# Kernel optimization log

Measured on AMD Instinct MI355X. Metric: run time of the kernel, lower is better.

Reference implementation:

```python
import jax, jax.numpy as jnp
import numpy as np

V = 32000   # vocab
D = 512     # embed dim
H = 512     # hidden dim
K = 5       # beam size
SOS, EOS, PAD = 0, 1, 2
NEG = -1e30  # acts as -inf but keeps grads NaN-free


def gru_cell(x, h, Wih, Whh, bih, bhh):
    # torch nn.GRU cell convention: gates ordered (r, z, n)
    gi = x @ Wih.T + bih
    gh = h @ Whh.T + bhh
    i_r, i_z, i_n = jnp.split(gi, 3, axis=-1)
    h_r, h_z, h_n = jnp.split(gh, 3, axis=-1)
    r = jax.nn.sigmoid(i_r + h_r)
    z = jax.nn.sigmoid(i_z + h_z)
    n = jnp.tanh(i_n + r * h_n)
    return (1.0 - z) * n + z * h


def setup_inputs() -> dict:
    key = jax.random.key(0)
    ks = jax.random.split(key, 14)
    s = 0.02
    f = jnp.float32
    return {
        "source": jax.random.randint(ks[0], (32, 32), 0, V, dtype=jnp.int32),
        "emb_src": jax.random.normal(ks[1], (V, D), f) * s,
        "emb_tgt": jax.random.normal(ks[2], (V, D), f) * s,
        "enc_Wih": jax.random.normal(ks[3], (3 * H, D), f) * s,
        "enc_Whh": jax.random.normal(ks[4], (3 * H, H), f) * s,
        "enc_bih": jnp.zeros((3 * H,), f),
        "enc_bhh": jnp.zeros((3 * H,), f),
        "dec_Wih": jax.random.normal(ks[5], (3 * H, D), f) * s,
        "dec_Whh": jax.random.normal(ks[6], (3 * H, H), f) * s,
        "dec_bih": jnp.zeros((3 * H,), f),
        "dec_bhh": jnp.zeros((3 * H,), f),
        "W_out": jax.random.normal(ks[7], (H, V), f) * s,
        "b_out": jnp.zeros((V,), f),
    }


def beam_search(source, emb_src, emb_tgt, enc_Wih, enc_Whh, enc_bih, enc_bhh,
                dec_Wih, dec_Whh, dec_bih, dec_bhh, W_out, b_out):
    B, S = source.shape
    T = S + 1  # max decode steps (while counter < source.shape[1] + 1)

    # ---- encoder: 1-layer GRU over source tokens ----
    xs = jnp.swapaxes(emb_src[source], 0, 1)  # [S, B, D]
    def enc_step(h, x):
        return gru_cell(x, h, enc_Wih, enc_Whh, enc_bih, enc_bhh), None
    h_enc, _ = jax.lax.scan(enc_step, jnp.zeros((B, H), xs.dtype), xs)
    # initialize_h: repeat each sentence's hidden state beam_size times
    hidden = jnp.broadcast_to(h_enc[:, None, :], (B, K, H))  # [B, K, H]

    def dec_logprobs(tok, hid):
        x = emb_tgt[tok]  # [B, K, D]
        h1 = gru_cell(x, hid, dec_Wih, dec_Whh, dec_bih, dec_bhh)
        lp = jax.nn.log_softmax(h1 @ W_out + b_out, axis=-1)  # [B, K, V]
        return lp, h1

    # ---- step 0: initial_advance (top-K words from one SOS row) ----
    lp, h1 = dec_logprobs(jnp.zeros((B, K), jnp.int32), hidden)
    vals, words = jax.lax.top_k(lp[:, 0, :], K)  # [B, K]
    seqs = jnp.full((B, K, T + 1), PAD, jnp.int32)
    seqs = seqs.at[:, :, 0].set(SOS).at[:, :, 1].set(words)
    act_ll = vals
    hidden = h1  # all beams identical at step 0
    best_ll = jnp.full((B,), NEG, vals.dtype)
    best_seq = jnp.full((B, T + 1), PAD, jnp.int32)
    pos = jnp.arange(T + 1)
    bidx = jnp.arange(B)

    # ---- steps 1..T-1: advance. Dead beam slots carry NEG likelihood,
    # which reproduces the shrinking-active-set math of the original. ----
    def step(carry, t):
        seqs, act_ll, hidden, last_tok, best_ll, best_seq = carry
        lp, h1 = dec_logprobs(last_tok, hidden)
        L = (act_ll[:, :, None] + lp).reshape(B, K * V)
        vals, idx = jax.lax.top_k(L, K)
        parent = idx // V           # seq_ind
        word = idx % V              # word_ind
        gathered = jnp.take_along_axis(seqs, parent[:, :, None], axis=1)
        new_seqs = jnp.where(pos[None, None, :] == t + 1, word[:, :, None], gathered)
        finite = vals > NEG * 0.5
        is_eos = (word == EOS) & finite
        # completed likelihood normalized by candidate length (t+2 tokens)
        comp_ll = jnp.where(is_eos, vals / (t.astype(vals.dtype) + 2.0), NEG)
        cbest = comp_ll.max(axis=1)
        cseq = new_seqs[bidx, comp_ll.argmax(axis=1)]  # [B, T+1], PAD-padded
        improve = cbest > best_ll
        best_ll = jnp.where(improve, cbest, best_ll)
        best_seq = jnp.where(improve[:, None], cseq, best_seq)
        act_ll = jnp.where(finite & ~is_eos, vals, NEG)
        hidden = jnp.take_along_axis(h1, parent[:, :, None], axis=1)  # arrange_h gather
        return (new_seqs, act_ll, hidden, word, best_ll, best_seq), None

    carry = (seqs, act_ll, hidden, words, best_ll, best_seq)
    carry, _ = jax.lax.scan(step, carry, jnp.arange(1, T))
    seqs, act_ll, hidden, last_tok, best_ll, best_seq = carry

    # return_winner: best completed if any, else best active
    have = best_ll > NEG * 0.5
    act_best = act_ll.argmax(axis=1)
    act_seq = seqs[bidx, act_best]
    winner = jnp.where(have[:, None], best_seq, act_seq)  # [B, T+1]
    winner_ll = jnp.where(have, best_ll, act_ll.max(axis=1))
    return winner, winner_ll


def reference(source, emb_src, emb_tgt, enc_Wih, enc_Whh, enc_bih, enc_bhh,
              dec_Wih, dec_Whh, dec_bih, dec_bhh, W_out, b_out):
    winner, _ = beam_search(source, emb_src, emb_tgt, enc_Wih, enc_Whh, enc_bih,
                            enc_bhh, dec_Wih, dec_Whh, dec_bih, dec_bhh, W_out, b_out)
    return winner
```

## Files before the change

kernel.cpp:

```cpp
#include <hip/hip_runtime.h>
#include <math.h>

#define NEGF   (-1e30f)
#define FINTH  (-5e29f)
#define VSZ    32000
#define KBM    5
#define SEQL   34
#define NVBLK  1000

__device__ __forceinline__ bool cand_gt(float av, int ai, float bv, int bi) {
  return (av > bv) || (av == bv && ai < bi);
}

#define INS5(xx, ii)                                                           \
  if (cand_gt(xx, ii, tv4, ti4)) {                                             \
    tv4 = xx; ti4 = ii;                                                        \
    if (cand_gt(tv4, ti4, tv3, ti3)) { float tf = tv3; int tj = ti3; tv3 = tv4; ti3 = ti4; tv4 = tf; ti4 = tj; \
      if (cand_gt(tv3, ti3, tv2, ti2)) { tf = tv2; tj = ti2; tv2 = tv3; ti2 = ti3; tv3 = tf; ti3 = tj; \
        if (cand_gt(tv2, ti2, tv1, ti1)) { tf = tv1; tj = ti1; tv1 = tv2; ti1 = ti2; tv2 = tf; ti2 = tj; \
          if (cand_gt(tv1, ti1, tv0, ti0)) { tf = tv0; tj = ti0; tv0 = tv1; ti0 = ti1; tv1 = tf; ti1 = tj; } } } } }

__global__ void init_kernel(float* hb0, int* word_buf, int* hsrc) {
  int i = blockIdx.x * 256 + threadIdx.x;
  if (i < 32 * 512) hb0[i] = 0.f;
  if (i < 160) { word_buf[i] = 0; hsrc[i] = i / KBM; }
}

__global__ __launch_bounds__(256, 4) void genc_kernel(
    const float* __restrict__ emb, const int* __restrict__ source,
    const float* __restrict__ Wih, float* __restrict__ gi_enc)
{
  const int tid = threadIdx.x;
  const int ng = tid & 7;
  const int mg = tid >> 3;
  const int j0 = blockIdx.x * 16 + ng * 2;
  const int r0 = blockIdx.y * 128 + mg * 4;

  const float* arow[4];
  #pragma unroll
  for (int i = 0; i < 4; i++) {
    int r = r0 + i;
    int tok = source[(r & 31) * 32 + (r >> 5)];
    arow[i] = emb + (long)tok * 512;
  }
  const float* w0p = Wih + (long)j0 * 512;
  const float* w1p = w0p + 512;

  float acc0[4], acc1[4];
  #pragma unroll
  for (int i = 0; i < 4; i++) { acc0[i] = 0.f; acc1[i] = 0.f; }

  float4 wc0 = *(const float4*)w0p;
  float4 wc1 = *(const float4*)w1p;
  float4 ac[4];
  #pragma unroll
  for (int i = 0; i < 4; i++) ac[i] = *(const float4*)arow[i];

  for (int k = 0; k < 508; k += 4) {
    float4 wn0 = *(const float4*)(w0p + k + 4);
    float4 wn1 = *(const float4*)(w1p + k + 4);
    float4 an[4];
    #pragma unroll
    for (int i = 0; i < 4; i++) an[i] = *(const float4*)(arow[i] + k + 4);
    #pragma unroll
    for (int i = 0; i < 4; i++) {
      acc0[i] += ac[i].x * wc0.x + ac[i].y * wc0.y + ac[i].z * wc0.z + ac[i].w * wc0.w;
      acc1[i] += ac[i].x * wc1.x + ac[i].y * wc1.y + ac[i].z * wc1.z + ac[i].w * wc1.w;
    }
    wc0 = wn0; wc1 = wn1;
    #pragma unroll
    for (int i = 0; i < 4; i++) ac[i] = an[i];
  }
  #pragma unroll
  for (int i = 0; i < 4; i++) {
    acc0[i] += ac[i].x * wc0.x + ac[i].y * wc0.y + ac[i].z * wc0.z + ac[i].w * wc0.w;
    acc1[i] += ac[i].x * wc1.x + ac[i].y * wc1.y + ac[i].z * wc1.z + ac[i].w * wc1.w;
  }
  #pragma unroll
  for (int i = 0; i < 4; i++) {
    float2 r; r.x = acc0[i]; r.y = acc1[i];
    *(float2*)(gi_enc + (long)(r0 + i) * 1536 + j0) = r;
  }
}

template<int P, int HONLY>
__global__ __launch_bounds__(256, 4) void gates_kernel(
    const float* __restrict__ emb, const int* __restrict__ tok_ptr, int tok_stride,
    const float* __restrict__ hbuf, const int* __restrict__ hsrc,
    const float* __restrict__ Wih, const float* __restrict__ Whh,
    float* __restrict__ gip, float* __restrict__ ghp)
{
  const bool is_h = HONLY ? true : (blockIdx.y != 0);
  const float* W = is_h ? Whh : Wih;
  const int M = 32 * P;
  float* out = (is_h ? ghp : gip) + (long)blockIdx.z * M * 1536;

  const int tid = threadIdx.x;
  const int ng = tid & 7;
  const int mg = tid >> 3;
  const int j0 = blockIdx.x * 16 + ng * 2;
  const int k0 = blockIdx.z * 128;

  const float* arow[P];
  #pragma unroll
  for (int i = 0; i < P; i++) {
    int m = mg * P + i;
    if (is_h) { int r = hsrc ? hsrc[m] : m; arow[i] = hbuf + (long)r * 512 + k0; }
    else      { int tk = tok_ptr[m * tok_stride]; arow[i] = emb + (long)tk * 512 + k0; }
  }
  const float* w0p = W + (long)j0 * 512 + k0;
  const float* w1p = w0p + 512;

  float acc0[P], acc1[P];
  #pragma unroll
  for (int i = 0; i < P; i++) { acc0[i] = 0.f; acc1[i] = 0.f; }

  float4 wc0 = *(const float4*)w0p;
  float4 wc1 = *(const float4*)w1p;
  float4 ac[P];
  #pragma unroll
  for (int i = 0; i < P; i++) ac[i] = *(const float4*)arow[i];

  for (int k = 0; k < 124; k += 4) {
    float4 wn0 = *(const float4*)(w0p + k + 4);
    float4 wn1 = *(const float4*)(w1p + k + 4);
    float4 an[P];
    #pragma unroll
    for (int i = 0; i < P; i++) an[i] = *(const float4*)(arow[i] + k + 4);
    #pragma unroll
    for (int i = 0; i < P; i++) {
      acc0[i] += ac[i].x * wc0.x + ac[i].y * wc0.y + ac[i].z * wc0.z + ac[i].w * wc0.w;
      acc1[i] += ac[i].x * wc1.x + ac[i].y * wc1.y + ac[i].z * wc1.z + ac[i].w * wc1.w;
    }
    wc0 = wn0; wc1 = wn1;
    #pragma unroll
    for (int i = 0; i < P; i++) ac[i] = an[i];
  }
  #pragma unroll
  for (int i = 0; i < P; i++) {
    acc0[i] += ac[i].x * wc0.x + ac[i].y * wc0.y + ac[i].z * wc0.z + ac[i].w * wc0.w;
    acc1[i] += ac[i].x * wc1.x + ac[i].y * wc1.y + ac[i].z * wc1.z + ac[i].w * wc1.w;
  }
  #pragma unroll
  for (int i = 0; i < P; i++) {
    int m = mg * P + i;
    float2 r; r.x = acc0[i]; r.y = acc1[i];
    *(float2*)(out + (long)m * 1536 + j0) = r;
  }
}

template<int NPI, int NPH, int M>
__global__ __launch_bounds__(256) void hupd_kernel(
    const float* __restrict__ gip, const float* __restrict__ ghp,
    const float* __restrict__ bih, const float* __restrict__ bhh,
    const float* __restrict__ hin, const int* __restrict__ hsrc,
    float* __restrict__ hout)
{
  int idx = blockIdx.x * 256 + threadIdx.x;
  if (idx >= M * 512) return;
  int m = idx >> 9, i = idx & 511;
  float ir = 0.f, iz = 0.f, inn = 0.f, hr = 0.f, hz = 0.f, hn = 0.f;
  #pragma unroll
  for (int p = 0; p < NPI; p++) {
    const float* g = gip + (long)p * M * 1536 + (long)m * 1536;
    ir += g[i]; iz += g[512 + i]; inn += g[1024 + i];
  }
  #pragma unroll
  for (int p = 0; p < NPH; p++) {
    const float* g = ghp + (long)p * M * 1536 + (long)m * 1536;
    hr += g[i]; hz += g[512 + i]; hn += g[1024 + i];
  }
  ir += bih[i]; iz += bih[512 + i]; inn += bih[1024 + i];
  hr += bhh[i]; hz += bhh[512 + i]; hn += bhh[1024 + i];
  float r = 1.f / (1.f + expf(-(ir + hr)));
  float z = 1.f / (1.f + expf(-(iz + hz)));
  float n = tanhf(inn + r * hn);
  int src = hsrc ? hsrc[m] : m;
  float h = hin[(long)src * 512 + i];
  hout[(long)m * 512 + i] = (1.f - z) * n + z * h;
}

__global__ __launch_bounds__(256, 4) void logtop_kernel(
    const float* __restrict__ h1, const float* __restrict__ Wout,
    const float* __restrict__ bout,
    float* __restrict__ pms, float* __restrict__ pv, int* __restrict__ pi)
{
  const int tid = threadIdx.x;
  const int ng = tid & 7;
  const int mg = tid >> 3;
  const int blk = blockIdx.x;
  const int v = blk * 32 + ng * 4;
  const int m0 = mg * 5;

  const float* a0 = h1 + (long)m0 * 512;
  const float* wp = Wout + v;

  float4 acc[5];
  #pragma unroll
  for (int i = 0; i < 5; i++) acc[i] = make_float4(0.f, 0.f, 0.f, 0.f);

  float4 wc[4], ac[5];
  #pragma unroll
  for (int j = 0; j < 4; j++) wc[j] = *(const float4*)(wp + (long)j * VSZ);
  #pragma unroll
  for (int i = 0; i < 5; i++) ac[i] = *(const float4*)(a0 + i * 512);

  for (int k = 0; k < 508; k += 4) {
    float4 wn[4], an[5];
    #pragma unroll
    for (int j = 0; j < 4; j++) wn[j] = *(const float4*)(wp + (long)(k + 4 + j) * VSZ);
    #pragma unroll
    for (int i = 0; i < 5; i++) an[i] = *(const float4*)(a0 + i * 512 + k + 4);
    #pragma unroll
    for (int i = 0; i < 5; i++) {
      acc[i].x += ac[i].x * wc[0].x + ac[i].y * wc[1].x + ac[i].z * wc[2].x + ac[i].w * wc[3].x;
      acc[i].y += ac[i].x * wc[0].y + ac[i].y * wc[1].y + ac[i].z * wc[2].y + ac[i].w * wc[3].y;
      acc[i].z += ac[i].x * wc[0].z + ac[i].y * wc[1].z + ac[i].z * wc[2].z + ac[i].w * wc[3].z;
      acc[i].w += ac[i].x * wc[0].w + ac[i].y * wc[1].w + ac[i].z * wc[2].w + ac[i].w * wc[3].w;
    }
    #pragma unroll
    for (int j = 0; j < 4; j++) wc[j] = wn[j];
    #pragma unroll
    for (int i = 0; i < 5; i++) ac[i] = an[i];
  }
  #pragma unroll
  for (int i = 0; i < 5; i++) {
    acc[i].x += ac[i].x * wc[0].x + ac[i].y * wc[1].x + ac[i].z * wc[2].x + ac[i].w * wc[3].x;
    acc[i].y += ac[i].x * wc[0].y + ac[i].y * wc[1].y + ac[i].z * wc[2].y + ac[i].w * wc[3].y;
    acc[i].z += ac[i].x * wc[0].z + ac[i].y * wc[1].z + ac[i].z * wc[2].z + ac[i].w * wc[3].z;
    acc[i].w += ac[i].x * wc[0].w + ac[i].y * wc[1].w + ac[i].z * wc[2].w + ac[i].w * wc[3].w;
  }

  __shared__ float L[160][33];
  float4 bb = *(const float4*)(bout + v);
  #pragma unroll
  for (int i = 0; i < 5; i++) {
    L[m0 + i][ng * 4 + 0] = acc[i].x + bb.x;
    L[m0 + i][ng * 4 + 1] = acc[i].y + bb.y;
    L[m0 + i][ng * 4 + 2] = acc[i].z + bb.z;
    L[m0 + i][ng * 4 + 3] = acc[i].w + bb.w;
  }
  __syncthreads();

  if (tid < 160) {
    float m = -3.4e38f, s = 0.f;
    float tv0 = -3.4e38f, tv1 = -3.4e38f, tv2 = -3.4e38f, tv3 = -3.4e38f, tv4 = -3.4e38f;
    int ti0 = 0x7fffffff, ti1 = 0x7fffffff, ti2 = 0x7fffffff, ti3 = 0x7fffffff, ti4 = 0x7fffffff;
    int base = blk * 32;
    for (int c = 0; c < 32; c++) {
      float x = L[tid][c];
      if (x > m) { s *= expf(m - x); m = x; }
      s += expf(x - m);
      INS5(x, base + c);
    }
    long o = (long)blk * 160 + tid;
    pms[o * 2 + 0] = m; pms[o * 2 + 1] = s;
    pv[o * 5 + 0] = tv0; pi[o * 5 + 0] = ti0;
    pv[o * 5 + 1] = tv1; pi[o * 5 + 1] = ti1;
    pv[o * 5 + 2] = tv2; pi[o * 5 + 2] = ti2;
    pv[o * 5 + 3] = tv3; pi[o * 5 + 3] = ti3;
    pv[o * 5 + 4] = tv4; pi[o * 5 + 4] = ti4;
  }
}

__global__ __launch_bounds__(256) void merge_kernel(
    const float* __restrict__ pms, const float* __restrict__ pv,
    const int* __restrict__ pi, float* __restrict__ lse,
    float* __restrict__ rv5, int* __restrict__ ri5)
{
  int row = blockIdx.x, tid = threadIdx.x;
  float m = -3.4e38f, s = 0.f;
  float tv0 = -3.4e38f, tv1 = -3.4e38f, tv2 = -3.4e38f, tv3 = -3.4e38f, tv4 = -3.4e38f;
  int ti0 = 0x7fffffff, ti1 = 0x7fffffff, ti2 = 0x7fffffff, ti3 = 0x7fffffff, ti4 = 0x7fffffff;

  for (int blk = tid; blk < NVBLK; blk += 256) {
    long o = (long)blk * 160 + row;
    float bm = pms[o * 2 + 0], bs = pms[o * 2 + 1];
    float nm = fmaxf(m, bm);
    s = s * expf(m - nm) + bs * expf(bm - nm);
    m = nm;
    float xv; int xi;
    xv = pv[o * 5 + 0]; xi = pi[o * 5 + 0]; INS5(xv, xi);
    xv = pv[o * 5 + 1]; xi = pi[o * 5 + 1]; INS5(xv, xi);
    xv = pv[o * 5 + 2]; xi = pi[o * 5 + 2]; INS5(xv, xi);
    xv = pv[o * 5 + 3]; xi = pi[o * 5 + 3]; INS5(xv, xi);
    xv = pv[o * 5 + 4]; xi = pi[o * 5 + 4]; INS5(xv, xi);
  }
  for (int mask = 1; mask < 64; mask <<= 1) {
    float om = __shfl_xor(m, mask, 64);
    float os = __shfl_xor(s, mask, 64);
    float nm = fmaxf(m, om);
    s = s * expf(m - nm) + os * expf(om - nm);
    m = nm;
  }
  __shared__ float sm[4], ss[4];
  __shared__ float sv[256 * 5];
  __shared__ int   si[256 * 5];
  if ((tid & 63) == 0) { sm[tid >> 6] = m; ss[tid >> 6] = s; }
  sv[tid * 5 + 0] = tv0; si[tid * 5 + 0] = ti0;
  sv[tid * 5 + 1] = tv1; si[tid * 5 + 1] = ti1;
  sv[tid * 5 + 2] = tv2; si[tid * 5 + 2] = ti2;
  sv[tid * 5 + 3] = tv3; si[tid * 5 + 3] = ti3;
  sv[tid * 5 + 4] = tv4; si[tid * 5 + 4] = ti4;
  __syncthreads();
  if (tid == 0) {
    float M2 = sm[0], S2 = ss[0];
    for (int w = 1; w < 4; w++) {
      float nm = fmaxf(M2, sm[w]);
      S2 = S2 * expf(M2 - nm) + ss[w] * expf(sm[w] - nm);
      M2 = nm;
    }
    lse[row] = M2 + logf(S2);
  }
  for (int str = 128; str >= 1; str >>= 1) {
    if (tid < str) {
      float* av = &sv[tid * 5];         int* ai = &si[tid * 5];
      float* bv = &sv[(tid + str) * 5]; int* bi = &si[(tid + str) * 5];
      float o0[5]; int o1[5];
      int i = 0, j = 0;
      #pragma unroll
      for (int o = 0; o < 5; o++) {
        float avv = av[i]; int aii = ai[i];
        float bvv = bv[j]; int bii = bi[j];
        bool ta = cand_gt(avv, aii, bvv, bii);
        o0[o] = ta ? avv : bvv; o1[o] = ta ? aii : bii;
        i += ta ? 1 : 0; j += ta ? 0 : 1;
      }
      #pragma unroll
      for (int o = 0; o < 5; o++) { av[o] = o0[o]; ai[o] = o1[o]; }
    }
    __syncthreads();
  }
  if (tid == 0) {
    #pragma unroll
    for (int o = 0; o < 5; o++) { rv5[row * 5 + o] = sv[o]; ri5[row * 5 + o] = si[o]; }
  }
}

__global__ void book0_kernel(const float* __restrict__ rv5, const int* __restrict__ ri5,
                             const float* __restrict__ lse,
                             int* __restrict__ seqs, float* __restrict__ act_ll,
                             int* __restrict__ word_buf, int* __restrict__ hsrc,
                             float* __restrict__ best_ll, int* __restrict__ best_seq)
{
  int b = blockIdx.x, tid = threadIdx.x;
  int row = b * KBM;
  float l = lse[row];
  if (tid < SEQL) {
    for (int j = 0; j < KBM; j++) {
      int w = ri5[row * 5 + j];
      seqs[(b * KBM + j) * SEQL + tid] = (tid == 0) ? 0 : (tid == 1 ? w : 2);
    }
    best_seq[b * SEQL + tid] = 2;
  }
  if (tid < KBM) {
    act_ll[b * KBM + tid] = rv5[row * 5 + tid] - l;
    word_buf[b * KBM + tid] = ri5[row * 5 + tid];
    hsrc[b * KBM + tid] = b * KBM + tid;
  }
  if (tid == 0) best_ll[b] = NEGF;
}

__global__ void book_kernel(const float* __restrict__ rv5, const int* __restrict__ ri5,
                            const float* __restrict__ lse,
                            const int* __restrict__ seqs_old, int* __restrict__ seqs_new,
                            float* __restrict__ act_ll, int* __restrict__ word_buf,
                            int* __restrict__ hsrc, float* __restrict__ best_ll,
                            int* __restrict__ best_seq, int t)
{
  int b = blockIdx.x, tid = threadIdx.x;
  __shared__ float sv5[5];
  __shared__ int   si5[5];
  if (tid == 0) {
    float tv0 = -3.4e38f, tv1 = -3.4e38f, tv2 = -3.4e38f, tv3 = -3.4e38f, tv4 = -3.4e38f;
    int ti0 = 0x7fffffff, ti1 = 0x7fffffff, ti2 = 0x7fffffff, ti3 = 0x7fffffff, ti4 = 0x7fffffff;
    for (int k = 0; k < KBM; k++) {
      int row = b * KBM + k;
      float a = act_ll[row], l = lse[row];
      #pragma unroll
      for (int j = 0; j < 5; j++) {
        float x = a + (rv5[row * 5 + j] - l);
        int id = k * VSZ + ri5[row * 5 + j];
        INS5(x, id);
      }
    }
    sv5[0] = tv0; si5[0] = ti0; sv5[1] = tv1; si5[1] = ti1;
    sv5[2] = tv2; si5[2] = ti2; sv5[3] = tv3; si5[3] = ti3;
    sv5[4] = tv4; si5[4] = ti4;
  }
  __syncthreads();

  __shared__ int ls[KBM][SEQL];
  float v[KBM]; int pr[KBM], wd[KBM];
  #pragma unroll
  for (int j = 0; j < KBM; j++) {
    v[j] = sv5[j];
    int id = si5[j];
    pr[j] = id / VSZ; wd[j] = id % VSZ;
  }
  #pragma unroll
  for (int j = 0; j < KBM; j++) {
    if (tid < SEQL) {
      int x = (tid == t + 1) ? wd[j] : seqs_old[(b * KBM + pr[j]) * SEQL + tid];
      ls[j][tid] = x;
      seqs_new[(b * KBM + j) * SEQL + tid] = x;
    }
  }
  __syncthreads();
  float cll[KBM];
  #pragma unroll
  for (int j = 0; j < KBM; j++) {
    bool fin = v[j] > FINTH;
    bool eos = (wd[j] == 1) && fin;
    cll[j] = eos ? v[j] / (float)(t + 2) : NEGF;
  }
  int jb = 0; float cb = cll[0];
  #pragma unroll
  for (int j = 1; j < KBM; j++) if (cll[j] > cb) { cb = cll[j]; jb = j; }
  bool improve = cb > best_ll[b];
  if (improve) {
    if (tid == 0) best_ll[b] = cb;
    if (tid < SEQL) best_seq[b * SEQL + tid] = ls[jb][tid];
  }
  if (tid < KBM) {
    int j = tid;
    bool fin = v[j] > FINTH;
    bool eos = (wd[j] == 1) && fin;
    act_ll[b * KBM + j] = (fin && !eos) ? v[j] : NEGF;
    word_buf[b * KBM + j] = wd[j];
    hsrc[b * KBM + j] = b * KBM + pr[j];
  }
}

__global__ void final_kernel(const float* __restrict__ best_ll, const int* __restrict__ best_seq,
                             const float* __restrict__ act_ll, const int* __restrict__ seqs,
                             int* __restrict__ out)
{
  int b = blockIdx.x, tid = threadIdx.x;
  bool have = best_ll[b] > FINTH;
  int jb = 0; float ab = act_ll[b * KBM];
  for (int j = 1; j < KBM; j++)
    if (act_ll[b * KBM + j] > ab) { ab = act_ll[b * KBM + j]; jb = j; }
  if (tid < SEQL)
    out[b * SEQL + tid] = have ? best_seq[b * SEQL + tid]
                               : seqs[(b * KBM + jb) * SEQL + tid];
}

extern "C" void kernel_launch(void* const* d_in, const int* in_sizes, int n_in,
                              void* d_out, int out_size, void* d_ws, size_t ws_size,
                              hipStream_t stream)
{
  const int*   source  = (const int*)d_in[0];
  const float* emb_src = (const float*)d_in[1];
  const float* emb_tgt = (const float*)d_in[2];
  const float* eWih = (const float*)d_in[3];
  const float* eWhh = (const float*)d_in[4];
  const float* ebih = (const float*)d_in[5];
  const float* ebhh = (const float*)d_in[6];
  const float* dWih = (const float*)d_in[7];
  const float* dWhh = (const float*)d_in[8];
  const float* dbih = (const float*)d_in[9];
  const float* dbhh = (const float*)d_in[10];
  const float* Wout = (const float*)d_in[11];
  const float* bout = (const float*)d_in[12];
  int* out = (int*)d_out;

  char* ws = (char*)d_ws;
  size_t off = 0;
  auto alloc = [&](size_t bytes) {
    void* p = ws + off;
    off = (off + bytes + 255) & ~(size_t)255;
    return p;
  };
  float* hb0     = (float*)alloc(160 * 512 * 4);
  float* hb1     = (float*)alloc(160 * 512 * 4);
  float* gip     = (float*)alloc((size_t)4 * 160 * 1536 * 4);
  float* ghp     = (float*)alloc((size_t)4 * 160 * 1536 * 4);
  char*  uni     = (char*) alloc((size_t)8 * 1024 * 1024);
  float* gi_enc  = (float*)uni;
  float* pms     = (float*)uni;
  float* pv      = (float*)(uni + 1536 * 1024);
  int*   pi      = (int*)  (uni + 1536 * 1024 + 3328 * 1024);
  float* lse     = (float*)alloc(160 * 4);
  float* act_ll  = (float*)alloc(160 * 4);
  float* rv5     = (float*)alloc(160 * 5 * 4);
  float* best_ll = (float*)alloc(32 * 4);
  int*   ri5     = (int*)alloc(160 * 5 * 4);
  int*   seqs0   = (int*)alloc(160 * SEQL * 4);
  int*   seqs1   = (int*)alloc(160 * SEQL * 4);
  int*   wordb   = (int*)alloc(160 * 4);
  int*   hsrc    = (int*)alloc(160 * 4);
  int*   bseq    = (int*)alloc(32 * SEQL * 4);

  init_kernel<<<64, 256, 0, stream>>>(hb0, wordb, hsrc);

  genc_kernel<<<dim3(96, 8), 256, 0, stream>>>(emb_src, source, eWih, gi_enc);
  for (int s = 0; s < 32; s++) {
    gates_kernel<1, 1><<<dim3(96, 1, 4), 256, 0, stream>>>(
        nullptr, nullptr, 0, hb0, nullptr, nullptr, eWhh, nullptr, ghp);
    hupd_kernel<1, 4, 32><<<64, 256, 0, stream>>>(
        gi_enc + (size_t)s * 32 * 1536, ghp, ebih, ebhh, hb0, nullptr, hb0);
  }

  gates_kernel<5, 0><<<dim3(96, 2, 4), 256, 0, stream>>>(
      emb_tgt, wordb, 1, hb0, hsrc, dWih, dWhh, gip, ghp);
  hupd_kernel<4, 4, 160><<<320, 256, 0, stream>>>(
      gip, ghp, dbih, dbhh, hb0, hsrc, hb1);
  logtop_kernel<<<NVBLK, 256, 0, stream>>>(hb1, Wout, bout, pms, pv, pi);
  merge_kernel<<<160, 256, 0, stream>>>(pms, pv, pi, lse, rv5, ri5);
  book0_kernel<<<32, 64, 0, stream>>>(rv5, ri5, lse, seqs0, act_ll, wordb, hsrc,
                                      best_ll, bseq);

  float* hcur = hb1; float* hoth = hb0;
  int* scur = seqs0; int* soth = seqs1;
  for (int t = 1; t <= 32; t++) {
    gates_kernel<5, 0><<<dim3(96, 2, 4), 256, 0, stream>>>(
        emb_tgt, wordb, 1, hcur, hsrc, dWih, dWhh, gip, ghp);
    hupd_kernel<4, 4, 160><<<320, 256, 0, stream>>>(
        gip, ghp, dbih, dbhh, hcur, hsrc, hoth);
    logtop_kernel<<<NVBLK, 256, 0, stream>>>(hoth, Wout, bout, pms, pv, pi);
    merge_kernel<<<160, 256, 0, stream>>>(pms, pv, pi, lse, rv5, ri5);
    book_kernel<<<32, 64, 0, stream>>>(rv5, ri5, lse, scur, soth, act_ll, wordb,
                                       hsrc, best_ll, bseq, t);
    { float* tmp = hcur; hcur = hoth; hoth = tmp; }
    { int* tmp = scur; scur = soth; soth = tmp; }
  }

  final_kernel<<<32, 64, 0, stream>>>(best_ll, bseq, act_ll, scur, out);
}
```

Measured before the change: 8.174 ms.

## Stage W_out tiles into LDS via async global_load_lds with double buffering

Reworks the logits matmul so W_out tiles (64 rows x 32 columns) are copied straight from global memory into a double-buffered shared-memory region with global_load_lds, instead of each thread loading its own float4 weight rows into registers. Threads then read the weights from LDS, while the activation rows are still prefetched from global with a two-step register ping-pong. The aim is to cut redundant global weight traffic across the 20 threads that share columns and to overlap the next tile's load with compute. In exchange it adds LDS use and a barrier per tile, which may lower occupancy. It also relies on the loads having completed by the time the barrier passes, with no explicit wait on the async copy.

```diff
diff --git a/kernel.cpp b/kernel.cpp
--- a/kernel.cpp
+++ b/kernel.cpp
@@ -189,56 +189,85 @@
   const int ng = tid & 7;
   const int mg = tid >> 3;
   const int blk = blockIdx.x;
-  const int v = blk * 32 + ng * 4;
+  const int v0 = blk * 32;
+  const int v = v0 + ng * 4;
   const int m0 = mg * 5;
 
+  __shared__ float Wlds[2][2048];
+  __shared__ float L[160][33];
+
   const float* a0 = h1 + (long)m0 * 512;
-  const float* wp = Wout + v;
+
+  const int skk = tid >> 3;
+  const int sv4 = tid & 7;
+  const float* sg0 = Wout + (size_t)skk * VSZ + v0 + sv4 * 4;
+  const float* sg1 = Wout + (size_t)(32 + skk) * VSZ + v0 + sv4 * 4;
+  const int lwave = (tid >> 6) * 256;
+
+  auto stage = [&](int tt, int bb) {
+    const float* g0 = sg0 + (size_t)tt * 64 * VSZ;
+    const float* g1 = sg1 + (size_t)tt * 64 * VSZ;
+    __builtin_amdgcn_global_load_lds(
+        (const __attribute__((address_space(1))) void*)g0,
+        (__attribute__((address_space(3))) void*)&Wlds[bb][lwave], 16, 0, 0);
+    __builtin_amdgcn_global_load_lds(
+        (const __attribute__((address_space(1))) void*)g1,
+        (__attribute__((address_space(3))) void*)&Wlds[bb][1024 + lwave], 16, 0, 0);
+  };
 
   float4 acc[5];
   #pragma unroll
   for (int i = 0; i < 5; i++) acc[i] = make_float4(0.f, 0.f, 0.f, 0.f);
 
-  float4 wc[4], ac[5];
-  #pragma unroll
-  for (int j = 0; j < 4; j++) wc[j] = *(const float4*)(wp + (long)j * VSZ);
-  #pragma unroll
-  for (int i = 0; i < 5; i++) ac[i] = *(const float4*)(a0 + i * 512);
-
-  for (int k = 0; k < 508; k += 4) {
-    float4 wn[4], an[5];
-    #pragma unroll
-    for (int j = 0; j < 4; j++) wn[j] = *(const float4*)(wp + (long)(k + 4 + j) * VSZ);
-    #pragma unroll
-    for (int i = 0; i < 5; i++) an[i] = *(const float4*)(a0 + i * 512 + k + 4);
-    #pragma unroll
-    for (int i = 0; i < 5; i++) {
-      acc[i].x += ac[i].x * wc[0].x + ac[i].y * wc[1].x + ac[i].z * wc[2].x + ac[i].w * wc[3].x;
-      acc[i].y += ac[i].x * wc[0].y + ac[i].y * wc[1].y + ac[i].z * wc[2].y + ac[i].w * wc[3].y;
-      acc[i].z += ac[i].x * wc[0].z + ac[i].y * wc[1].z + ac[i].z * wc[2].z + ac[i].w * wc[3].z;
-      acc[i].w += ac[i].x * wc[0].w + ac[i].y * wc[1].w + ac[i].z * wc[2].w + ac[i].w * wc[3].w;
-    }
-    #pragma unroll
-    for (int j = 0; j < 4; j++) wc[j] = wn[j];
-    #pragma unroll
-    for (int i = 0; i < 5; i++) ac[i] = an[i];
-  }
+  stage(0, 0);
+  __syncthreads();
+
+  float4 aA[5], aB[5];
+  #pragma unroll
+  for (int i = 0; i < 5; i++) aA[i] = *(const float4*)(a0 + i * 512);
+
+  for (int t8 = 0; t8 < 8; t8++) {
+    const float* lb = &Wlds[t8 & 1][0];
+    if (t8 < 7) stage(t8 + 1, (t8 + 1) & 1);
+    const int kt = t8 * 64;
+    #pragma unroll 1
+    for (int c = 0; c < 16; c += 2) {
+      const int k = kt + c * 4;
+      float4 w0[4], w1[4];
+      #pragma unroll
+      for (int j = 0; j < 4; j++) w0[j] = *(const float4*)&lb[(c * 4 + j) * 32 + ng * 4];
+      #pragma unroll
+      for (int j = 0; j < 4; j++) w1[j] = *(const float4*)&lb[(c * 4 + 4 + j) * 32 + ng * 4];
+      #pragma unroll
+      for (int i = 0; i < 5; i++) aB[i] = *(const float4*)(a0 + i * 512 + k + 4);
+      #pragma unroll
+      for (int i = 0; i < 5; i++) {
+        acc[i].x += aA[i].x * w0[0].x + aA[i].y * w0[1].x + aA[i].z * w0[2].x + aA[i].w * w0[3].x;
+        acc[i].y += aA[i].x * w0[0].y + aA[i].y * w0[1].y + aA[i].z * w0[2].y + aA[i].w * w0[3].y;
+        acc[i].z += aA[i].x * w0[0].z + aA[i].y * w0[1].z + aA[i].z * w0[2].z + aA[i].w * w0[3].z;
+        acc[i].w += aA[i].x * w0[0].w + aA[i].y * w0[1].w + aA[i].z * w0[2].w + aA[i].w * w0[3].w;
+      }
+      int kn = k + 8; if (kn >= 512) kn = 0;
+      #pragma unroll
+      for (int i = 0; i < 5; i++) aA[i] = *(const float4*)(a0 + i * 512 + kn);
+      #pragma unroll
+      for (int i = 0; i < 5; i++) {
+        acc[i].x += aB[i].x * w1[0].x + aB[i].y * w1[1].x + aB[i].z * w1[2].x + aB[i].w * w1[3].x;
+        acc[i].y += aB[i].x * w1[0].y + aB[i].y * w1[1].y + aB[i].z * w1[2].y + aB[i].w * w1[3].y;
+        acc[i].z += aB[i].x * w1[0].z + aB[i].y * w1[1].z + aB[i].z * w1[2].z + aB[i].w * w1[3].z;
+        acc[i].w += aB[i].x * w1[0].w + aB[i].y * w1[1].w + aB[i].z * w1[2].w + aB[i].w * w1[3].w;
+      }
+    }
+    __syncthreads();
+  }
+
+  float4 bb4 = *(const float4*)(bout + v);
   #pragma unroll
   for (int i = 0; i < 5; i++) {
-    acc[i].x += ac[i].x * wc[0].x + ac[i].y * wc[1].x + ac[i].z * wc[2].x + ac[i].w * wc[3].x;
-    acc[i].y += ac[i].x * wc[0].y + ac[i].y * wc[1].y + ac[i].z * wc[2].y + ac[i].w * wc[3].y;
-    acc[i].z += ac[i].x * wc[0].z + ac[i].y * wc[1].z + ac[i].z * wc[2].z + ac[i].w * wc[3].z;
-    acc[i].w += ac[i].x * wc[0].w + ac[i].y * wc[1].w + ac[i].z * wc[2].w + ac[i].w * wc[3].w;
-  }
-
-  __shared__ float L[160][33];
-  float4 bb = *(const float4*)(bout + v);
-  #pragma unroll
-  for (int i = 0; i < 5; i++) {
-    L[m0 + i][ng * 4 + 0] = acc[i].x + bb.x;
-    L[m0 + i][ng * 4 + 1] = acc[i].y + bb.y;
-    L[m0 + i][ng * 4 + 2] = acc[i].z + bb.z;
-    L[m0 + i][ng * 4 + 3] = acc[i].w + bb.w;
+    L[m0 + i][ng * 4 + 0] = acc[i].x + bb4.x;
+    L[m0 + i][ng * 4 + 1] = acc[i].y + bb4.y;
+    L[m0 + i][ng * 4 + 2] = acc[i].z + bb4.z;
+    L[m0 + i][ng * 4 + 3] = acc[i].w + bb4.w;
   }
   __syncthreads();
 
```

After: 6.886 ms. 15.8% less time.
